# Kernel optimization log

Measured on AMD Instinct MI355X. Metric: run time of the kernel, lower is better.

The kernel has to match this reference:

```python
import jax, jax.numpy as jnp
import numpy as np

NGROUP, CIN, COUT, K, HIDDEN = 8, 16, 16, 5, True


def _build_mask():
    # Group-causal PixelCNN-style mask for a 5x5 kernel.
    # Spatial: rows above center fully visible; center row visible left of center.
    # Center tap: input group g_in visible to output group g_out iff
    #   g_in <= g_out (hidden layer) or g_in < g_out (input layer).
    nout, cinall = NGROUP * COUT, NGROUP * CIN
    c = K // 2
    m = np.zeros((nout, cinall, K, K), dtype=np.float32)
    m[:, :, :c, :] = 1.0          # rows strictly above center
    m[:, :, c, :c] = 1.0          # center row, left of center
    g_out = np.arange(nout)[:, None] // COUT   # (nout,1)
    g_in = np.arange(cinall)[None, :] // CIN   # (1,cinall)
    center_ok = (g_in <= g_out) if HIDDEN else (g_in < g_out)
    m[:, :, c, c] = center_ok.astype(np.float32)
    return jnp.asarray(m)

_MASK = _build_mask()


def setup_inputs() -> dict:
    key = jax.random.key(0)
    k1, k2 = jax.random.split(key)
    x = jax.random.normal(k1, (8, 128, 256, 512), dtype=jnp.float32)
    weight = jax.random.uniform(k2, (128, 128, 5, 5), dtype=jnp.float32)
    bias = jnp.zeros((128,), dtype=jnp.float32)
    slope = jnp.zeros((128,), dtype=jnp.float32)  # PReLU slope (zero -> ReLU)
    return {"x": x, "weight": weight, "bias": bias, "slope": slope}


def reference(x, weight, bias, slope):
    w = weight * _MASK  # apply causal group mask
    # context pad by 2 then valid 5x5 conv == SAME padding conv
    y = jax.lax.conv_general_dilated(
        x, w, window_strides=(1, 1), padding=((2, 2), (2, 2)),
        dimension_numbers=("NCHW", "OIHW", "NCHW"))
    y = y + bias[None, :, None, None]
    a = slope[None, :, None, None]
    return jnp.where(y > 0, y, a * y)  # per-channel PReLU
```

## Files before the change

kernel.cpp:

```cpp
#include <hip/hip_runtime.h>
#include <hip/hip_bf16.h>

typedef __attribute__((ext_vector_type(8))) short short8;
typedef __attribute__((ext_vector_type(4))) float f32x4;

#define CH 128
#define H 256
#define W 512
#define PH 258
#define PW 516
#define NTAPS 13
#define P_BYTES (PH * PW * CH * 2)
#define P_SHORTS (PH * PW * CH)
#define CHW (CH * H * W)

#define GRAN_PER_ROW 544
#define NLOADS 52
#define BUF_SHORTS (3328 * 8)
#define ROW_SHORTS (136 * 32)

#define GLD_LDS16(g, l)                                                        \
  __builtin_amdgcn_global_load_lds(                                            \
      (const __attribute__((address_space(1))) void*)(g),                      \
      (__attribute__((address_space(3))) void*)(l), 16, 0, 0)

__global__ void zero_pads(unsigned int* __restrict__ Pd) {
    int row  = blockIdx.x;
    int slab = blockIdx.y;
    unsigned int* base = Pd + (size_t)slab * (P_SHORTS / 2);
    int tid = threadIdx.x;
    if (row < 2) {
        unsigned int* r = base + (size_t)row * (PW * 64);
        for (int i = tid; i < PW * 64; i += 256) r[i] = 0u;
    } else {
        int seg = tid >> 6;
        int col = seg < 2 ? seg : 512 + seg;
        base[((size_t)row * PW + col) * 64 + (tid & 63)] = 0u;
    }
}

__global__ void premask_weights(const float* __restrict__ w,
                                __hip_bfloat16* __restrict__ Wt2) {
    int idx  = blockIdx.x * 256 + threadIdx.x;
    int frag = idx >> 9;
    int r    = idx & 511;
    int l    = r >> 3;
    int e    = r & 7;
    int t    = frag >> 5;
    int ob   = (frag >> 2) & 7;
    int kcg  = frag & 3;
    int oc   = ob * 16 + (l & 15);
    int ic   = kcg * 32 + (l >> 4) * 8 + e;
    int ky   = t < 5 ? 0 : (t < 10 ? 1 : 2);
    int kx   = t - ky * 5;
    float v  = w[(oc * CH + ic) * 25 + ky * 5 + kx];
    if (t == 12 && ((ic >> 4) > (oc >> 4))) v = 0.f;
    Wt2[idx] = __float2bfloat16(v);
}

__global__ void transpose_pad_all(const float* __restrict__ x,
                                  __hip_bfloat16* __restrict__ Pbase) {
    __shared__ float tile[32][33];
    const float* xn = x + (size_t)blockIdx.z * CHW;
    unsigned short* P = (unsigned short*)(Pbase + (size_t)blockIdx.z * P_SHORTS);
    int h  = blockIdx.y;
    int wt = blockIdx.x & 15;
    int ct = blockIdx.x >> 4;
    int tx = threadIdx.x & 31;
    int ty = threadIdx.x >> 5;
#pragma unroll
    for (int r = 0; r < 4; ++r) {
        int c = ct * 32 + ty + r * 8;
        tile[ty + r * 8][tx] = xn[(c * H + h) * W + wt * 32 + tx];
    }
    __syncthreads();
    int wl = threadIdx.x >> 3;
    int cq = threadIdx.x & 7;
    union { ushort4 u; __hip_bfloat16 hh[4]; } v;
    v.hh[0] = __float2bfloat16(tile[cq * 4 + 0][wl]);
    v.hh[1] = __float2bfloat16(tile[cq * 4 + 1][wl]);
    v.hh[2] = __float2bfloat16(tile[cq * 4 + 2][wl]);
    v.hh[3] = __float2bfloat16(tile[cq * 4 + 3][wl]);
    *reinterpret_cast<ushort4*>(
        P + ((size_t)(h + 2) * PW + (wt * 32 + wl + 2)) * CH + ct * 32 + cq * 4) = v.u;
}

__global__ __launch_bounds__(512, 2)
void conv_mfma_all(const __hip_bfloat16* __restrict__ Pbase,
                   const __hip_bfloat16* __restrict__ Wt2,
                   const float* __restrict__ bias,
                   const float* __restrict__ slope,
                   float* __restrict__ out) {
    __shared__ short lds[2 * BUF_SHORTS];
    const __hip_bfloat16* P = Pbase + (size_t)blockIdx.z * P_SHORTS;
    float* outn = out + (size_t)blockIdx.z * CHW;
    int h0    = blockIdx.y << 2;
    int w0    = blockIdx.x << 7;
    int tid   = threadIdx.x;
    int lane  = tid & 63;
    int wv    = tid >> 6;
    int l15   = lane & 15;
    int khi   = lane >> 4;
    int obf   = (wv & 1) * 4;
    int hsel  = wv >> 1;

    f32x4 acc[4][8];
#pragma unroll
    for (int mi = 0; mi < 4; ++mi)
#pragma unroll
        for (int ni = 0; ni < 8; ++ni)
            acc[mi][ni] = (f32x4){0.f, 0.f, 0.f, 0.f};

    const short* Wt2s = (const short*)Wt2;

    int stoff[7];
#pragma unroll
    for (int i = 0; i < 7; ++i) {
        int s    = wv + i * 8;
        int g64  = (s << 6) + lane;
        int row  = (g64 >= 544) + (g64 >= 1088) + (g64 >= 1632) +
                   (g64 >= 2176) + (g64 >= 2720);
        int rem  = g64 - row * GRAN_PER_ROW;
        int px   = rem >> 2;
        int chk  = rem & 3;
        int pxc  = px < 132 ? px : 131;
        int ccs  = chk ^ (pxc & 3);
        stoff[i] = ((h0 + row) * PW + (w0 + pxc)) * CH + ccs * 8;
    }
    int bq[5];
#pragma unroll
    for (int kx = 0; kx < 5; ++kx) {
        int pxb = kx + l15;
        bq[kx] = (pxb * 4 + (khi ^ (pxb & 3))) * 8;
    }

    auto stage = [&](int kk, int b) {
#pragma unroll
        for (int i = 0; i < 7; ++i) {
            int s = wv + i * 8;
            if (s < NLOADS)
                GLD_LDS16(P + stoff[i] + kk * 32,
                          (char*)lds + b * (BUF_SHORTS * 2) + (s << 10));
        }
    };

    stage(0, 0);
    __syncthreads();

    for (int kk = 0; kk < 4; ++kk) {
        int cur = kk & 1;
        if (kk < 3) stage(kk + 1, cur ^ 1);

        const short* apb = Wt2s + ((obf * 4 + kk) << 9) + (lane << 3);
        const short* bb  = lds + cur * BUF_SHORTS + hsel * ROW_SHORTS;
#pragma unroll
        for (int t = 0; t < NTAPS; ++t) {
            int ky  = t < 5 ? 0 : (t < 10 ? 1 : 2);
            int kx  = t - ky * 5;
            const short* ap = apb + t * 16384;
            const short* bp = bb + ky * ROW_SHORTS + bq[kx];
            short8 a[4], b[8];
#pragma unroll
            for (int mi = 0; mi < 4; ++mi)
                a[mi] = *reinterpret_cast<const short8*>(ap + mi * 2048);
#pragma unroll
            for (int ni = 0; ni < 8; ++ni)
                b[ni] = *reinterpret_cast<const short8*>(bp + ni * 512);
            __builtin_amdgcn_s_setprio(1);
#pragma unroll
            for (int mi = 0; mi < 4; ++mi)
#pragma unroll
                for (int ni = 0; ni < 8; ++ni)
                    acc[mi][ni] = __builtin_amdgcn_mfma_f32_16x16x32_bf16(
                        a[mi], b[ni], acc[mi][ni], 0, 0, 0);
            __builtin_amdgcn_s_setprio(0);
        }
        __syncthreads();
    }

    int hrow = h0 + hsel;
#pragma unroll
    for (int mi = 0; mi < 4; ++mi) {
        int ocb = obf * 16 + mi * 16 + 4 * khi;
        f32x4 b4 = *reinterpret_cast<const f32x4*>(bias + ocb);
        f32x4 s4 = *reinterpret_cast<const f32x4*>(slope + ocb);
#pragma unroll
        for (int i = 0; i < 4; ++i) {
            float* orow = outn + ((ocb + i) * H + hrow) * W + w0;
#pragma unroll
            for (int ni = 0; ni < 8; ++ni) {
                float v = acc[mi][ni][i] + b4[i];
                v = v > 0.f ? v : s4[i] * v;
                orow[ni * 16 + l15] = v;
            }
        }
    }
}

extern "C" void kernel_launch(void* const* d_in, const int* in_sizes, int n_in,
                              void* d_out, int out_size, void* d_ws, size_t ws_size,
                              hipStream_t stream) {
    const float* x      = (const float*)d_in[0];
    const float* weight = (const float*)d_in[1];
    const float* bias   = (const float*)d_in[2];
    const float* slope  = (const float*)d_in[3];
    float* out = (float*)d_out;

    __hip_bfloat16* Pbase = (__hip_bfloat16*)d_ws;
    __hip_bfloat16* Wt2   = (__hip_bfloat16*)((char*)d_ws + 8 * (size_t)P_BYTES);

    zero_pads<<<dim3(PH, 8), 256, 0, stream>>>((unsigned int*)d_ws);
    premask_weights<<<832, 256, 0, stream>>>(weight, Wt2);
    transpose_pad_all<<<dim3(64, 256, 8), 256, 0, stream>>>(x, Pbase);
    conv_mfma_all<<<dim3(4, 64, 8), 512, 0, stream>>>(Pbase, Wt2, bias, slope, out);
}
```

Baseline: 592.0 us.

## Halve conv block height, shrink per-wave tile, and re-swizzle LDS pixel layout

Measured after the change: 640.3 us. 1.08x slower.

```diff
diff --git a/kernel.cpp b/kernel.cpp
--- a/kernel.cpp
+++ b/kernel.cpp
@@ -15,9 +15,9 @@
 #define CHW (CH * H * W)
 
 #define GRAN_PER_ROW 544
-#define NLOADS 52
-#define BUF_SHORTS (3328 * 8)
-#define ROW_SHORTS (136 * 32)
+#define NLOADS 34
+#define TILE_SHORTS (4 * GRAN_PER_ROW * 8)
+#define ROW_SHORTS (GRAN_PER_ROW * 8)
 
 #define GLD_LDS16(g, l)                                                        \
   __builtin_amdgcn_global_load_lds(                                            \
@@ -85,62 +85,58 @@
         P + ((size_t)(h + 2) * PW + (wt * 32 + wl + 2)) * CH + ct * 32 + cq * 4) = v.u;
 }
 
-__global__ __launch_bounds__(512, 2)
+__global__ __launch_bounds__(512, 4)
 void conv_mfma_all(const __hip_bfloat16* __restrict__ Pbase,
                    const __hip_bfloat16* __restrict__ Wt2,
                    const float* __restrict__ bias,
                    const float* __restrict__ slope,
                    float* __restrict__ out) {
-    __shared__ short lds[2 * BUF_SHORTS];
+    __shared__ short lds[2 * TILE_SHORTS];
     const __hip_bfloat16* P = Pbase + (size_t)blockIdx.z * P_SHORTS;
     float* outn = out + (size_t)blockIdx.z * CHW;
-    int h0    = blockIdx.y << 2;
-    int w0    = blockIdx.x << 7;
-    int tid   = threadIdx.x;
-    int lane  = tid & 63;
-    int wv    = tid >> 6;
-    int l15   = lane & 15;
-    int khi   = lane >> 4;
-    int obf   = (wv & 1) * 4;
-    int hsel  = wv >> 1;
-
-    f32x4 acc[4][8];
+    int h0   = blockIdx.y << 1;
+    int w0   = blockIdx.x << 7;
+    int tid  = threadIdx.x;
+    int lane = tid & 63;
+    int wv   = tid >> 6;
+    int l15  = lane & 15;
+    int khi  = lane >> 4;
+    int ohf  = wv & 1;
+    int pxh  = (wv >> 1) & 1;
+    int hsel = wv >> 2;
+
+    f32x4 acc[4][4];
 #pragma unroll
     for (int mi = 0; mi < 4; ++mi)
 #pragma unroll
-        for (int ni = 0; ni < 8; ++ni)
+        for (int ni = 0; ni < 4; ++ni)
             acc[mi][ni] = (f32x4){0.f, 0.f, 0.f, 0.f};
 
     const short* Wt2s = (const short*)Wt2;
 
-    int stoff[7];
-#pragma unroll
-    for (int i = 0; i < 7; ++i) {
+    int stoff[5];
+#pragma unroll
+    for (int i = 0; i < 5; ++i) {
         int s    = wv + i * 8;
-        int g64  = (s << 6) + lane;
-        int row  = (g64 >= 544) + (g64 >= 1088) + (g64 >= 1632) +
-                   (g64 >= 2176) + (g64 >= 2720);
-        int rem  = g64 - row * GRAN_PER_ROW;
-        int px   = rem >> 2;
-        int chk  = rem & 3;
+        int ss   = s < NLOADS ? s : NLOADS - 1;
+        int g64  = (ss << 6) + lane;
+        int row  = (g64 >= 544) + (g64 >= 1088) + (g64 >= 1632);
+        int G    = g64 - row * GRAN_PER_ROW;
+        int pair = G >> 3;
+        int qd   = (G & 7) ^ (pair & 7);
+        int px   = pair * 2 + (qd >> 2);
+        int chk  = qd & 3;
         int pxc  = px < 132 ? px : 131;
-        int ccs  = chk ^ (pxc & 3);
-        stoff[i] = ((h0 + row) * PW + (w0 + pxc)) * CH + ccs * 8;
-    }
-    int bq[5];
-#pragma unroll
-    for (int kx = 0; kx < 5; ++kx) {
-        int pxb = kx + l15;
-        bq[kx] = (pxb * 4 + (khi ^ (pxb & 3))) * 8;
-    }
-
-    auto stage = [&](int kk, int b) {
-#pragma unroll
-        for (int i = 0; i < 7; ++i) {
+        stoff[i] = ((h0 + row) * PW + (w0 + pxc)) * CH + chk * 8;
+    }
+
+    auto stage = [&](int kk, int bsel) {
+#pragma unroll
+        for (int i = 0; i < 5; ++i) {
             int s = wv + i * 8;
             if (s < NLOADS)
                 GLD_LDS16(P + stoff[i] + kk * 32,
-                          (char*)lds + b * (BUF_SHORTS * 2) + (s << 10));
+                          (char*)lds + bsel * (TILE_SHORTS * 2) + (s << 10));
         }
     };
 
@@ -148,29 +144,31 @@
     __syncthreads();
 
     for (int kk = 0; kk < 4; ++kk) {
-        int cur = kk & 1;
+        const int cur = kk & 1;
         if (kk < 3) stage(kk + 1, cur ^ 1);
 
-        const short* apb = Wt2s + ((obf * 4 + kk) << 9) + (lane << 3);
-        const short* bb  = lds + cur * BUF_SHORTS + hsel * ROW_SHORTS;
+        const short* bb = lds + cur * TILE_SHORTS + hsel * ROW_SHORTS;
 #pragma unroll
         for (int t = 0; t < NTAPS; ++t) {
-            int ky  = t < 5 ? 0 : (t < 10 ? 1 : 2);
-            int kx  = t - ky * 5;
-            const short* ap = apb + t * 16384;
-            const short* bp = bb + ky * ROW_SHORTS + bq[kx];
-            short8 a[4], b[8];
+            const int ky = t < 5 ? 0 : (t < 10 ? 1 : 2);
+            const int kx = t - ky * 5;
+            const short* ap = Wt2s + ((t * 32 + ohf * 16 + kk) << 9) + (lane << 3);
+            int p   = pxh * 64 + kx + l15;
+            int pr  = p >> 1;
+            int inr = (((p & 1) << 2) | khi) ^ (pr & 7);
+            const short* bp = bb + ky * ROW_SHORTS + ((pr << 3) + inr) * 8;
+            short8 a[4], b[4];
 #pragma unroll
             for (int mi = 0; mi < 4; ++mi)
                 a[mi] = *reinterpret_cast<const short8*>(ap + mi * 2048);
 #pragma unroll
-            for (int ni = 0; ni < 8; ++ni)
+            for (int ni = 0; ni < 4; ++ni)
                 b[ni] = *reinterpret_cast<const short8*>(bp + ni * 512);
             __builtin_amdgcn_s_setprio(1);
 #pragma unroll
             for (int mi = 0; mi < 4; ++mi)
 #pragma unroll
-                for (int ni = 0; ni < 8; ++ni)
+                for (int ni = 0; ni < 4; ++ni)
                     acc[mi][ni] = __builtin_amdgcn_mfma_f32_16x16x32_bf16(
                         a[mi], b[ni], acc[mi][ni], 0, 0, 0);
             __builtin_amdgcn_s_setprio(0);
@@ -181,14 +179,14 @@
     int hrow = h0 + hsel;
 #pragma unroll
     for (int mi = 0; mi < 4; ++mi) {
-        int ocb = obf * 16 + mi * 16 + 4 * khi;
+        int ocb = ohf * 64 + mi * 16 + 4 * khi;
         f32x4 b4 = *reinterpret_cast<const f32x4*>(bias + ocb);
         f32x4 s4 = *reinterpret_cast<const f32x4*>(slope + ocb);
 #pragma unroll
         for (int i = 0; i < 4; ++i) {
-            float* orow = outn + ((ocb + i) * H + hrow) * W + w0;
-#pragma unroll
-            for (int ni = 0; ni < 8; ++ni) {
+            float* orow = outn + ((ocb + i) * H + hrow) * W + w0 + pxh * 64;
+#pragma unroll
+            for (int ni = 0; ni < 4; ++ni) {
                 float v = acc[mi][ni][i] + b4[i];
                 v = v > 0.f ? v : s4[i] * v;
                 orow[ni * 16 + l15] = v;
@@ -212,5 +210,5 @@
     zero_pads<<<dim3(PH, 8), 256, 0, stream>>>((unsigned int*)d_ws);
     premask_weights<<<832, 256, 0, stream>>>(weight, Wt2);
     transpose_pad_all<<<dim3(64, 256, 8), 256, 0, stream>>>(x, Pbase);
-    conv_mfma_all<<<dim3(4, 64, 8), 512, 0, stream>>>(Pbase, Wt2, bias, slope, out);
-}
+    conv_mfma_all<<<dim3(4, 128, 8), 512, 0, stream>>>(Pbase, Wt2, bias, slope, out);
+}
```
